# Kernel tuning notes

Measured on AMD Instinct MI355X. Metric: run time of the kernel, lower is better.

Reference implementation:

```python
import jax, jax.numpy as jnp
import numpy as np

N = 50000      # nodes
E = 800000     # edges (before self-loops)
D_IN = 256     # input feature dim
H = 4          # attention heads
C = 32         # per-head channels
HID = H * C    # 128, concat output dim
BN_EPS = 1e-5


def setup_inputs() -> dict:
    key = jax.random.key(0)
    ks = jax.random.split(key, 24)
    inp = {}
    inp["x"] = jax.random.normal(ks[0], (N, D_IN), jnp.float32)
    inp["edge_index"] = jax.random.randint(ks[1], (2, E), 0, N, jnp.int32)
    # layer 1 GATConv params
    inp["W1"] = jax.random.normal(ks[2], (D_IN, HID), jnp.float32) * (2.0 / (D_IN + HID)) ** 0.5
    inp["att_src1"] = jax.random.normal(ks[3], (H, C), jnp.float32) * 0.1
    inp["att_dst1"] = jax.random.normal(ks[4], (H, C), jnp.float32) * 0.1
    inp["bias1"] = jnp.zeros((HID,), jnp.float32)
    # layer 1 BatchNorm (eval mode)
    inp["gamma1"] = 1.0 + 0.1 * jax.random.normal(ks[5], (HID,), jnp.float32)
    inp["beta1"] = 0.1 * jax.random.normal(ks[6], (HID,), jnp.float32)
    inp["mean1"] = 0.1 * jax.random.normal(ks[7], (HID,), jnp.float32)
    inp["var1"] = 0.5 + jax.random.uniform(ks[8], (HID,), jnp.float32)
    # layer 2 GATConv params
    inp["W2"] = jax.random.normal(ks[9], (HID, HID), jnp.float32) * (2.0 / (HID + HID)) ** 0.5
    inp["att_src2"] = jax.random.normal(ks[10], (H, C), jnp.float32) * 0.1
    inp["att_dst2"] = jax.random.normal(ks[11], (H, C), jnp.float32) * 0.1
    inp["bias2"] = jnp.zeros((HID,), jnp.float32)
    # layer 2 BatchNorm (eval mode)
    inp["gamma2"] = 1.0 + 0.1 * jax.random.normal(ks[12], (HID,), jnp.float32)
    inp["beta2"] = 0.1 * jax.random.normal(ks[13], (HID,), jnp.float32)
    inp["mean2"] = 0.1 * jax.random.normal(ks[14], (HID,), jnp.float32)
    inp["var2"] = 0.5 + jax.random.uniform(ks[15], (HID,), jnp.float32)
    return inp


def _gat_layer(x, src, dst, W, att_src, att_dst, bias):
    # x: [N, D]; src/dst: [Etot] with self-loops already appended
    h = (x @ W).reshape(N, H, C)                       # [N, H, C]
    a_s = jnp.einsum("nhc,hc->nh", h, att_src)         # [N, H]
    a_d = jnp.einsum("nhc,hc->nh", h, att_dst)         # [N, H]
    e = jax.nn.leaky_relu(a_s[src] + a_d[dst], 0.2)    # [Etot, H]
    # edge softmax over incoming edges of each destination node
    m = jax.ops.segment_max(e, dst, num_segments=N)    # [N, H]
    ex = jnp.exp(e - m[dst])                           # [Etot, H]
    den = jax.ops.segment_sum(ex, dst, num_segments=N) # [N, H]
    alpha = ex / (den[dst] + 1e-16)                    # [Etot, H]
    out = jax.ops.segment_sum(h[src] * alpha[:, :, None], dst, num_segments=N)
    return out.reshape(N, HID) + bias                  # concat heads + bias


def _bn_eval(x, gamma, beta, mean, var):
    return (x - mean) * (gamma * jax.lax.rsqrt(var + BN_EPS)) + beta


def reference(x, edge_index, W1, att_src1, att_dst1, bias1, gamma1, beta1, mean1, var1,
              W2, att_src2, att_dst2, bias2, gamma2, beta2, mean2, var2):
    loop = jnp.arange(N, dtype=edge_index.dtype)
    src = jnp.concatenate([edge_index[0], loop])  # PyG GATConv adds self-loops
    dst = jnp.concatenate([edge_index[1], loop])
    h = _gat_layer(x, src, dst, W1, att_src1, att_dst1, bias1)
    h = jax.nn.relu(_bn_eval(h, gamma1, beta1, mean1, var1))  # dropout = identity (eval)
    h = _gat_layer(h, src, dst, W2, att_src2, att_dst2, bias2)
    h = jax.nn.relu(_bn_eval(h, gamma2, beta2, mean2, var2))
    return h
```

## Files before the change

### kernel.cpp

```cpp
#include <hip/hip_runtime.h>
#include <math.h>

#define N_NODES 50000
#define EDGES   800000
#define ETOT    (EDGES + N_NODES)
#define HID     128
#define NH      4

typedef __attribute__((ext_vector_type(8))) short short8;
typedef __attribute__((ext_vector_type(4))) float floatx4;

__device__ inline unsigned short f2bf(float f) {
    unsigned int u = __float_as_uint(f);
    u = u + 0x7FFFu + ((u >> 16) & 1u);
    return (unsigned short)(u >> 16);
}

#define NB 391
#define BCAP 2688
#define CHUNK 4096
#define BIN_BLOCKS ((ETOT + CHUNK - 1) / CHUNK)

__global__ __launch_bounds__(256) void init_cursor_kernel(int* __restrict__ cursor) {
    int t = blockIdx.x * 256 + threadIdx.x;
    if (t < NB) cursor[t] = t * BCAP;
}

__global__ __launch_bounds__(256) void bin_scatter_kernel(const int* __restrict__ ei,
                                                          int* __restrict__ cursor,
                                                          int* __restrict__ binned) {
    __shared__ int histL[NB];
    int t = threadIdx.x;
    for (int b = t; b < NB; b += 256) histL[b] = 0;
    __syncthreads();
    int base = blockIdx.x * CHUNK;
#pragma unroll
    for (int j = 0; j < 16; j++) {
        int e = base + j * 256 + t;
        if (e < ETOT) {
            int d = (e < EDGES) ? ei[EDGES + e] : (e - EDGES);
            atomicAdd(&histL[d >> 7], 1);
        }
    }
    __syncthreads();
    for (int b = t; b < NB; b += 256) {
        int c = histL[b];
        histL[b] = c ? atomicAdd(&cursor[b], c) : 0;
    }
    __syncthreads();
#pragma unroll
    for (int j = 0; j < 16; j++) {
        int e = base + j * 256 + t;
        if (e < ETOT) {
            int s, d;
            if (e < EDGES) { s = ei[e]; d = ei[EDGES + e]; }
            else           { s = d = e - EDGES; }
            int bb = d >> 7;
            int pos = atomicAdd(&histL[bb], 1);
            if (pos < (bb + 1) * BCAP)
                binned[pos] = (s << 7) | (d & 127);
        }
    }
}

__global__ __launch_bounds__(256) void bin_finalize_kernel(const int* __restrict__ binned,
                                                           const int* __restrict__ cursor,
                                                           int* __restrict__ starts,
                                                           int* __restrict__ degs,
                                                           int* __restrict__ csr) {
    __shared__ int histN[128];
    __shared__ int excl[128];
    int b = blockIdx.x, t = threadIdx.x;
    int n0 = b << 7;
    int S = b * BCAP;
    int cnt = cursor[b] - S;
    if (cnt > BCAP) cnt = BCAP;
    if (t < 128) histN[t] = 0;
    __syncthreads();
    for (int j = t; j < cnt; j += 256)
        atomicAdd(&histN[binned[S + j] & 127], 1);
    __syncthreads();
    int v = (t < 128) ? histN[t] : 0;
    if (t < 128) excl[t] = v;
    __syncthreads();
    for (int off = 1; off < 128; off <<= 1) {
        int x = 0, add = 0;
        if (t < 128) { x = excl[t]; if (t >= off) add = excl[t - off]; }
        __syncthreads();
        if (t < 128) excl[t] = x + add;
        __syncthreads();
    }
    if (t < 128) {
        int ex = excl[t] - v;
        int n = n0 + t;
        if (n < N_NODES) { starts[n] = S + ex; degs[n] = v; }
        histN[t] = ex;
    }
    __syncthreads();
    for (int j = t; j < cnt; j += 256) {
        int e = binned[S + j];
        int pos = atomicAdd(&histN[e & 127], 1);
        csr[S + pos] = e >> 7;
    }
}

__global__ void wtrans_coef_kernel(const float* __restrict__ W1, const float* __restrict__ W2,
                                   unsigned short* __restrict__ Wt1, unsigned short* __restrict__ Wt2,
                                   const float* __restrict__ b1, const float* __restrict__ g1,
                                   const float* __restrict__ be1, const float* __restrict__ mn1,
                                   const float* __restrict__ vr1,
                                   const float* __restrict__ b2, const float* __restrict__ g2,
                                   const float* __restrict__ be2, const float* __restrict__ mn2,
                                   const float* __restrict__ vr2, float* __restrict__ coef) {
    int i = blockIdx.x * 256 + threadIdx.x;
    if (i < 256 * 128) { int k = i >> 7, n = i & 127; Wt1[n * 256 + k] = f2bf(W1[i]); }
    if (i < 128 * 128) { int k = i >> 7, n = i & 127; Wt2[n * 128 + k] = f2bf(W2[i]); }
    if (blockIdx.x == 0) {
        int t = threadIdx.x;
        if (t < 128) {
            float sc = g1[t] * rsqrtf(vr1[t] + 1e-5f);
            coef[t]       = sc;
            coef[128 + t] = be1[t] + (b1[t] - mn1[t]) * sc;
        } else {
            int c = t - 128;
            float sc = g2[c] * rsqrtf(vr2[c] + 1e-5f);
            coef[256 + c] = sc;
            coef[384 + c] = be2[c] + (b2[c] - mn2[c]) * sc;
        }
    }
}

#define GR   64
#define KC   64
#define PADK 88
#define PADH 136

union Smem {
    struct { unsigned short Xs[GR][PADK]; unsigned short Ws[HID][PADK]; } s;
    unsigned short Hs[GR][PADH];
};

template<bool XBF16>
__global__ __launch_bounds__(256) void gemm_att_kernel(const void* __restrict__ Xv,
                                                       const unsigned short* __restrict__ Wt,
                                                       const float* __restrict__ att_src,
                                                       const float* __restrict__ att_dst,
                                                       unsigned short* __restrict__ Hout,
                                                       float* __restrict__ aS,
                                                       float* __restrict__ aD, int K) {
    __shared__ Smem sm;
    int t = threadIdx.x, lane = t & 63, w = t >> 6;
    int quad = lane >> 4, nl = lane & 15;
    int rowBase = blockIdx.x * GR;

    floatx4 acc[8];
    floatx4 zero = {0.f, 0.f, 0.f, 0.f};
#pragma unroll
    for (int b = 0; b < 8; b++) acc[b] = zero;

    const float*          Xf = (const float*)Xv;
    const unsigned short* Xb = (const unsigned short*)Xv;

    for (int k0 = 0; k0 < K; k0 += KC) {
#pragma unroll
        for (int it = 0; it < 2; it++) {
            int s5 = t + it * 256;
            int row = s5 >> 3, kg = s5 & 7;
            int gr = rowBase + row;
            unsigned short tmp[8];
            if (XBF16) {
                uint4 v = make_uint4(0, 0, 0, 0);
                if (gr < N_NODES) v = *(const uint4*)&Xb[(unsigned)(gr * K + k0 + kg * 8)];
                *(uint4*)tmp = v;
            } else {
                float4 v0 = make_float4(0, 0, 0, 0), v1 = v0;
                if (gr < N_NODES) {
                    const float* p = &Xf[(unsigned)(gr * K + k0 + kg * 8)];
                    v0 = *(const float4*)p;
                    v1 = *(const float4*)(p + 4);
                }
                tmp[0] = f2bf(v0.x); tmp[1] = f2bf(v0.y); tmp[2] = f2bf(v0.z); tmp[3] = f2bf(v0.w);
                tmp[4] = f2bf(v1.x); tmp[5] = f2bf(v1.y); tmp[6] = f2bf(v1.z); tmp[7] = f2bf(v1.w);
            }
            *(uint4*)&sm.s.Xs[row][kg * 8] = *(uint4*)tmp;
        }
#pragma unroll
        for (int it = 0; it < 4; it++) {
            int s5 = t + it * 256;
            int n = s5 >> 3, kg = s5 & 7;
            *(uint4*)&sm.s.Ws[n][kg * 8] = *(const uint4*)&Wt[(unsigned)(n * K + k0 + kg * 8)];
        }
        __syncthreads();
#pragma unroll
        for (int ks = 0; ks < 2; ks++) {
            int kb = ks * 32 + quad * 8;
            short8 a0 = *(const short8*)&sm.s.Xs[w * 16 + nl][kb];
#pragma unroll
            for (int ct = 0; ct < 8; ct++) {
                short8 b = *(const short8*)&sm.s.Ws[ct * 16 + nl][kb];
                acc[ct] = __builtin_amdgcn_mfma_f32_16x16x32_bf16(a0, b, acc[ct], 0, 0, 0);
            }
        }
        __syncthreads();
    }

#pragma unroll
    for (int ct = 0; ct < 8; ct++)
#pragma unroll
        for (int r = 0; r < 4; r++)
            sm.Hs[w * 16 + quad * 4 + r][ct * 16 + nl] = f2bf(acc[ct][r]);

    float asv[8], adv[8];
    {
        const float* ap = &att_src[nl * 8];
        const float* dp = &att_dst[nl * 8];
        *(float4*)&asv[0] = *(const float4*)ap;  *(float4*)&asv[4] = *(const float4*)(ap + 4);
        *(float4*)&adv[0] = *(const float4*)dp;  *(float4*)&adv[4] = *(const float4*)(dp + 4);
    }
    int hd = nl >> 2;
#pragma unroll
    for (int it = 0; it < 4; it++) {
        int rl = w * 16 + it * 4 + quad;
        int grow = rowBase + rl;
        uint4 v = *(const uint4*)&sm.Hs[rl][nl * 8];
        float f[8];
        f[0] = __uint_as_float(v.x << 16); f[1] = __uint_as_float(v.x & 0xffff0000u);
        f[2] = __uint_as_float(v.y << 16); f[3] = __uint_as_float(v.y & 0xffff0000u);
        f[4] = __uint_as_float(v.z << 16); f[5] = __uint_as_float(v.z & 0xffff0000u);
        f[6] = __uint_as_float(v.w << 16); f[7] = __uint_as_float(v.w & 0xffff0000u);
        float ds = 0.f, dd = 0.f;
#pragma unroll
        for (int j = 0; j < 8; j++) {
            ds = fmaf(f[j], asv[j], ds);
            dd = fmaf(f[j], adv[j], dd);
        }
        ds += __shfl_xor(ds, 1); ds += __shfl_xor(ds, 2);
        dd += __shfl_xor(dd, 1); dd += __shfl_xor(dd, 2);
        if (grow < N_NODES) {
            *(uint4*)&Hout[(unsigned)(grow * HID + nl * 8)] = v;
            if ((nl & 3) == 0) { aS[grow * 4 + hd] = ds; aD[grow * 4 + hd] = dd; }
        }
    }
}

#define ECAP 64

__device__ __forceinline__ void prefetch16(unsigned (&buf)[16], int srcreg,
                                           const char* hbase, int lane4) {
#pragma unroll
    for (int u = 0; u < 16; u++) {
        int s = __builtin_amdgcn_readlane(srcreg, u);
        buf[u] = *(const unsigned int*)(hbase + (((long)s) << 8) + lane4);
    }
}

__device__ __forceinline__ void consume16(const unsigned (&buf)[16], float xr,
                                          int abase, float& acc0, float& acc1) {
#pragma unroll
    for (int u = 0; u < 16; u++) {
        float au = __uint_as_float((unsigned)__builtin_amdgcn_ds_bpermute(
                        abase | (u << 2), (int)__float_as_uint(xr)));
        unsigned vv = buf[u];
        acc0 = fmaf(__uint_as_float(vv << 16),         au, acc0);
        acc1 = fmaf(__uint_as_float(vv & 0xffff0000u), au, acc1);
    }
}

template<bool OUTBF16>
__global__ __launch_bounds__(256) void gather_kernel(const unsigned short* __restrict__ hfeat,
                                                     const float* __restrict__ a_s,
                                                     const float* __restrict__ a_d,
                                                     const int* __restrict__ starts,
                                                     const int* __restrict__ degs,
                                                     const int* __restrict__ csr,
                                                     const float* __restrict__ coefA,
                                                     const float* __restrict__ coefB,
                                                     void* __restrict__ outv) {
    int t = threadIdx.x, lane = t & 63, ws = t >> 6;
    int h = lane >> 4, l16 = lane & 15;
    int n = blockIdx.x * 4 + ws;
    int start = starts[n];
    int deg = degs[n];
    float adh = a_d[(unsigned)(n * 4 + h)];
    int lane4 = lane << 2;
    int abase = (lane & 48) << 2;
    const char* hbase = (const char*)hfeat;

    int sreg[4];
#pragma unroll
    for (int it = 0; it < 4; it++) {
        int j = l16 + it * 16;
        sreg[it] = (j < deg) ? csr[start + j] : 0;
    }
    float e[4];
#pragma unroll
    for (int it = 0; it < 4; it++) {
        int j = l16 + it * 16;
        e[it] = -1e30f;
        if (j < deg) {
            float as = a_s[(unsigned)(sreg[it] * 4 + h)];
            float v = as + adh;
            e[it] = v > 0.f ? v : 0.2f * v;
        }
    }

    int cap = deg < ECAP ? deg : ECAP;
    unsigned vA[16], vB[16];
    prefetch16(vA, sreg[0], hbase, lane4);
    if (cap > 16) prefetch16(vB, sreg[1], hbase, lane4);

    float m = fmaxf(fmaxf(e[0], e[1]), fmaxf(e[2], e[3]));
    for (int j = ECAP + l16; j < deg; j += 16) {
        int s = csr[start + j];
        float as = a_s[(unsigned)(s * 4 + h)];
        float v = as + adh; v = v > 0.f ? v : 0.2f * v;
        m = fmaxf(m, v);
    }
#pragma unroll
    for (int off = 1; off < 16; off <<= 1) m = fmaxf(m, __shfl_xor(m, off));

    float x[4];
    float d = 0.f;
#pragma unroll
    for (int it = 0; it < 4; it++) { x[it] = __expf(e[it] - m); d += x[it]; }
    for (int j = ECAP + l16; j < deg; j += 16) {
        int s = csr[start + j];
        float as = a_s[(unsigned)(s * 4 + h)];
        float v = as + adh; v = v > 0.f ? v : 0.2f * v;
        d += __expf(v - m);
    }
#pragma unroll
    for (int off = 1; off < 16; off <<= 1) d += __shfl_xor(d, off);
    float rd = 1.0f / (d + 1e-16f);
    float xr[4];
#pragma unroll
    for (int it = 0; it < 4; it++) xr[it] = x[it] * rd;

    float acc0 = 0.f, acc1 = 0.f;
    consume16(vA, xr[0], abase, acc0, acc1);
    if (cap > 16) {
        if (cap > 32) prefetch16(vA, sreg[2], hbase, lane4);
        consume16(vB, xr[1], abase, acc0, acc1);
        if (cap > 32) {
            if (cap > 48) prefetch16(vB, sreg[3], hbase, lane4);
            consume16(vA, xr[2], abase, acc0, acc1);
            if (cap > 48) consume16(vB, xr[3], abase, acc0, acc1);
        }
    }
    for (int j = ECAP; j < deg; j++) {
        int s = csr[start + j];
        float as = a_s[(unsigned)(s * 4 + h)];
        float v2 = as + adh; v2 = v2 > 0.f ? v2 : 0.2f * v2;
        float al = __expf(v2 - m) * rd;
        unsigned int v = *(const unsigned int*)(hbase + (unsigned)((s << 8) + lane4));
        acc0 = fmaf(__uint_as_float(v << 16),         al, acc0);
        acc1 = fmaf(__uint_as_float(v & 0xffff0000u), al, acc1);
    }

    int c = lane * 2;
    float2 cA = *(const float2*)&coefA[c];
    float2 cB = *(const float2*)&coefB[c];
    float o0 = fmaxf(fmaf(acc0, cA.x, cB.x), 0.f);
    float o1 = fmaxf(fmaf(acc1, cA.y, cB.y), 0.f);
    if (OUTBF16) {
        unsigned int pk = (unsigned int)f2bf(o0) | ((unsigned int)f2bf(o1) << 16);
        ((unsigned int*)outv)[(unsigned)(n * 64 + lane)] = pk;
    } else {
        ((float2*)outv)[(unsigned)(n * 64 + lane)] = make_float2(o0, o1);
    }
}

extern "C" void kernel_launch(void* const* d_in, const int* in_sizes, int n_in,
                              void* d_out, int out_size, void* d_ws, size_t ws_size,
                              hipStream_t stream) {
    const float* x    = (const float*)d_in[0];
    const int*   ei   = (const int*)d_in[1];
    const float* W1   = (const float*)d_in[2];
    const float* as1  = (const float*)d_in[3];
    const float* ad1  = (const float*)d_in[4];
    const float* b1   = (const float*)d_in[5];
    const float* g1   = (const float*)d_in[6];
    const float* be1  = (const float*)d_in[7];
    const float* mn1  = (const float*)d_in[8];
    const float* vr1  = (const float*)d_in[9];
    const float* W2   = (const float*)d_in[10];
    const float* as2  = (const float*)d_in[11];
    const float* ad2  = (const float*)d_in[12];
    const float* b2   = (const float*)d_in[13];
    const float* g2   = (const float*)d_in[14];
    const float* be2  = (const float*)d_in[15];
    const float* mn2  = (const float*)d_in[16];
    const float* vr2  = (const float*)d_in[17];
    float* out = (float*)d_out;

    unsigned short* hb  = (unsigned short*)d_ws;
    unsigned short* x2b = hb + (size_t)N_NODES * HID;
    unsigned short* Wt1 = x2b + (size_t)N_NODES * HID;
    unsigned short* Wt2 = Wt1 + 128 * 256;
    float* aS    = (float*)(Wt2 + 128 * 128);
    float* aD    = aS + N_NODES * NH;
    float* coef  = aD + N_NODES * NH;
    int* cursor  = (int*)(coef + 512);
    int* starts  = cursor + NB;
    int* degs    = starts + N_NODES;
    int* binned  = degs + N_NODES;
    int* csr     = binned + NB * BCAP;

    init_cursor_kernel<<<2, 256, 0, stream>>>(cursor);
    bin_scatter_kernel<<<BIN_BLOCKS, 256, 0, stream>>>(ei, cursor, binned);
    bin_finalize_kernel<<<NB, 256, 0, stream>>>(binned, cursor, starts, degs, csr);
    wtrans_coef_kernel<<<128, 256, 0, stream>>>(W1, W2, Wt1, Wt2,
                                                b1, g1, be1, mn1, vr1,
                                                b2, g2, be2, mn2, vr2, coef);

    int gemmGrid = (N_NODES + GR - 1) / GR;
    int nodeGrid = N_NODES / 4;

    gemm_att_kernel<false><<<gemmGrid, 256, 0, stream>>>(x, Wt1, as1, ad1, hb, aS, aD, 256);
    gather_kernel<true><<<nodeGrid, 256, 0, stream>>>(hb, aS, aD, starts, degs, csr,
                                                      coef, coef + 128, (void*)x2b);
    gemm_att_kernel<true><<<gemmGrid, 256, 0, stream>>>(x2b, Wt2, as2, ad2, hb, aS, aD, 128);
    gather_kernel<false><<<nodeGrid, 256, 0, stream>>>(hb, aS, aD, starts, degs, csr,
                                                       coef + 256, coef + 384, (void*)out);
}
```

Baseline: 261.2 us.

## Widen gather loads to 16B, register-prefetch GEMM tiles, cache dst in binning

The gather kernel now has each lane load 16 bytes (8 bf16 channels) per source row instead of 4 bytes. Four lane-groups each handle a subset of the edges, and partial sums are combined with cross-group shuffles before the output is written. The GEMM kernel double-buffers global loads in registers so the next K-tile's loads overlap the current MFMA work. The binning kernel keeps destination indices in registers between its two passes, so they are not reloaded. These changes cut the number of memory instructions and expose latency hiding, at the cost of more registers and extra shuffle reductions.

```diff
diff --git a/kernel.cpp b/kernel.cpp
--- a/kernel.cpp
+++ b/kernel.cpp
@@ -34,13 +34,14 @@
     for (int b = t; b < NB; b += 256) histL[b] = 0;
     __syncthreads();
     int base = blockIdx.x * CHUNK;
+    int dreg[16];
 #pragma unroll
     for (int j = 0; j < 16; j++) {
         int e = base + j * 256 + t;
-        if (e < ETOT) {
-            int d = (e < EDGES) ? ei[EDGES + e] : (e - EDGES);
-            atomicAdd(&histL[d >> 7], 1);
-        }
+        int d = -1;
+        if (e < ETOT) d = (e < EDGES) ? ei[EDGES + e] : (e - EDGES);
+        dreg[j] = d;
+        if (d >= 0) atomicAdd(&histL[d >> 7], 1);
     }
     __syncthreads();
     for (int b = t; b < NB; b += 256) {
@@ -50,11 +51,10 @@
     __syncthreads();
 #pragma unroll
     for (int j = 0; j < 16; j++) {
-        int e = base + j * 256 + t;
-        if (e < ETOT) {
-            int s, d;
-            if (e < EDGES) { s = ei[e]; d = ei[EDGES + e]; }
-            else           { s = d = e - EDGES; }
+        int d = dreg[j];
+        if (d >= 0) {
+            int e = base + j * 256 + t;
+            int s = (e < EDGES) ? ei[e] : (e - EDGES);
             int bb = d >> 7;
             int pos = atomicAdd(&histL[bb], 1);
             if (pos < (bb + 1) * BCAP)
@@ -161,17 +161,20 @@
     const float*          Xf = (const float*)Xv;
     const unsigned short* Xb = (const unsigned short*)Xv;
 
-    for (int k0 = 0; k0 < K; k0 += KC) {
+    uint4  xu[2];
+    float4 xf[2][2];
+    uint4  wu[4];
+
+    auto LOADX = [&](int k0) {
 #pragma unroll
         for (int it = 0; it < 2; it++) {
             int s5 = t + it * 256;
             int row = s5 >> 3, kg = s5 & 7;
             int gr = rowBase + row;
-            unsigned short tmp[8];
             if (XBF16) {
                 uint4 v = make_uint4(0, 0, 0, 0);
                 if (gr < N_NODES) v = *(const uint4*)&Xb[(unsigned)(gr * K + k0 + kg * 8)];
-                *(uint4*)tmp = v;
+                xu[it] = v;
             } else {
                 float4 v0 = make_float4(0, 0, 0, 0), v1 = v0;
                 if (gr < N_NODES) {
@@ -179,18 +182,41 @@
                     v0 = *(const float4*)p;
                     v1 = *(const float4*)(p + 4);
                 }
+                xf[it][0] = v0; xf[it][1] = v1;
+            }
+        }
+    };
+    auto LOADW = [&](int k0) {
+#pragma unroll
+        for (int it = 0; it < 4; it++) {
+            int s5 = t + it * 256;
+            int nn = s5 >> 3, kg = s5 & 7;
+            wu[it] = *(const uint4*)&Wt[(unsigned)(nn * K + k0 + kg * 8)];
+        }
+    };
+    auto STORE = [&]() {
+#pragma unroll
+        for (int it = 0; it < 2; it++) {
+            int s5 = t + it * 256;
+            int row = s5 >> 3, kg = s5 & 7;
+            if (XBF16) {
+                *(uint4*)&sm.s.Xs[row][kg * 8] = xu[it];
+            } else {
+                unsigned short tmp[8];
+                float4 v0 = xf[it][0], v1 = xf[it][1];
                 tmp[0] = f2bf(v0.x); tmp[1] = f2bf(v0.y); tmp[2] = f2bf(v0.z); tmp[3] = f2bf(v0.w);
                 tmp[4] = f2bf(v1.x); tmp[5] = f2bf(v1.y); tmp[6] = f2bf(v1.z); tmp[7] = f2bf(v1.w);
+                *(uint4*)&sm.s.Xs[row][kg * 8] = *(uint4*)tmp;
             }
-            *(uint4*)&sm.s.Xs[row][kg * 8] = *(uint4*)tmp;
         }
 #pragma unroll
         for (int it = 0; it < 4; it++) {
             int s5 = t + it * 256;
-            int n = s5 >> 3, kg = s5 & 7;
-            *(uint4*)&sm.s.Ws[n][kg * 8] = *(const uint4*)&Wt[(unsigned)(n * K + k0 + kg * 8)];
-        }
-        __syncthreads();
+            int nn = s5 >> 3, kg = s5 & 7;
+            *(uint4*)&sm.s.Ws[nn][kg * 8] = wu[it];
+        }
+    };
+    auto MFMAC = [&]() {
 #pragma unroll
         for (int ks = 0; ks < 2; ks++) {
             int kb = ks * 32 + quad * 8;
@@ -201,8 +227,20 @@
                 acc[ct] = __builtin_amdgcn_mfma_f32_16x16x32_bf16(a0, b, acc[ct], 0, 0, 0);
             }
         }
+    };
+
+    LOADX(0); LOADW(0);
+    STORE();
+    __syncthreads();
+    for (int k0 = KC; k0 < K; k0 += KC) {
+        LOADX(k0); LOADW(k0);
+        MFMAC();
         __syncthreads();
-    }
+        STORE();
+        __syncthreads();
+    }
+    MFMAC();
+    __syncthreads();
 
 #pragma unroll
     for (int ct = 0; ct < 8; ct++)
@@ -245,24 +283,30 @@
 
 #define ECAP 64
 
-__device__ __forceinline__ void prefetch16(unsigned (&buf)[16], int srcreg,
-                                           const char* hbase, int lane4) {
-#pragma unroll
-    for (int u = 0; u < 16; u++) {
-        int s = __builtin_amdgcn_readlane(srcreg, u);
-        buf[u] = *(const unsigned int*)(hbase + (((long)s) << 8) + lane4);
-    }
-}
-
-__device__ __forceinline__ void consume16(const unsigned (&buf)[16], float xr,
-                                          int abase, float& acc0, float& acc1) {
-#pragma unroll
-    for (int u = 0; u < 16; u++) {
+__device__ __forceinline__ void prefetchR(uint4 (&buf)[4], int sregr, const char* hbase,
+                                          int sBase, int l16b) {
+#pragma unroll
+    for (int u = 0; u < 4; u++) {
+        int se = __builtin_amdgcn_ds_bpermute(sBase | (u << 2), sregr);
+        buf[u] = *(const uint4*)(hbase + (((long)se) << 8) + l16b);
+    }
+}
+
+__device__ __forceinline__ void consumeR(const uint4 (&buf)[4], float xrr, int aBase,
+                                         float (&acc)[8]) {
+#pragma unroll
+    for (int u = 0; u < 4; u++) {
         float au = __uint_as_float((unsigned)__builtin_amdgcn_ds_bpermute(
-                        abase | (u << 2), (int)__float_as_uint(xr)));
-        unsigned vv = buf[u];
-        acc0 = fmaf(__uint_as_float(vv << 16),         au, acc0);
-        acc1 = fmaf(__uint_as_float(vv & 0xffff0000u), au, acc1);
+                        aBase | (u << 2), (int)__float_as_uint(xrr)));
+        uint4 v = buf[u];
+        acc[0] = fmaf(__uint_as_float(v.x << 16),         au, acc[0]);
+        acc[1] = fmaf(__uint_as_float(v.x & 0xffff0000u), au, acc[1]);
+        acc[2] = fmaf(__uint_as_float(v.y << 16),         au, acc[2]);
+        acc[3] = fmaf(__uint_as_float(v.y & 0xffff0000u), au, acc[3]);
+        acc[4] = fmaf(__uint_as_float(v.z << 16),         au, acc[4]);
+        acc[5] = fmaf(__uint_as_float(v.z & 0xffff0000u), au, acc[5]);
+        acc[6] = fmaf(__uint_as_float(v.w << 16),         au, acc[6]);
+        acc[7] = fmaf(__uint_as_float(v.w & 0xffff0000u), au, acc[7]);
     }
 }
 
@@ -282,9 +326,10 @@
     int start = starts[n];
     int deg = degs[n];
     float adh = a_d[(unsigned)(n * 4 + h)];
-    int lane4 = lane << 2;
-    int abase = (lane & 48) << 2;
     const char* hbase = (const char*)hfeat;
+    int sBase = lane & 48;
+    int aBase = ((lane & 12) << 4) | sBase;
+    int l16b = l16 << 4;
 
     int sreg[4];
 #pragma unroll
@@ -305,9 +350,9 @@
     }
 
     int cap = deg < ECAP ? deg : ECAP;
-    unsigned vA[16], vB[16];
-    prefetch16(vA, sreg[0], hbase, lane4);
-    if (cap > 16) prefetch16(vB, sreg[1], hbase, lane4);
+    uint4 vA[4], vB[4];
+    prefetchR(vA, sreg[0], hbase, sBase, l16b);
+    if (cap > 16) prefetchR(vB, sreg[1], hbase, sBase, l16b);
 
     float m = fmaxf(fmaxf(e[0], e[1]), fmaxf(e[2], e[3]));
     for (int j = ECAP + l16; j < deg; j += 16) {
@@ -336,37 +381,64 @@
 #pragma unroll
     for (int it = 0; it < 4; it++) xr[it] = x[it] * rd;
 
-    float acc0 = 0.f, acc1 = 0.f;
-    consume16(vA, xr[0], abase, acc0, acc1);
+    float acc[8];
+#pragma unroll
+    for (int j = 0; j < 8; j++) acc[j] = 0.f;
+    consumeR(vA, xr[0], aBase, acc);
     if (cap > 16) {
-        if (cap > 32) prefetch16(vA, sreg[2], hbase, lane4);
-        consume16(vB, xr[1], abase, acc0, acc1);
+        if (cap > 32) prefetchR(vA, sreg[2], hbase, sBase, l16b);
+        consumeR(vB, xr[1], aBase, acc);
         if (cap > 32) {
-            if (cap > 48) prefetch16(vB, sreg[3], hbase, lane4);
-            consume16(vA, xr[2], abase, acc0, acc1);
-            if (cap > 48) consume16(vB, xr[3], abase, acc0, acc1);
-        }
-    }
-    for (int j = ECAP; j < deg; j++) {
-        int s = csr[start + j];
-        float as = a_s[(unsigned)(s * 4 + h)];
-        float v2 = as + adh; v2 = v2 > 0.f ? v2 : 0.2f * v2;
-        float al = __expf(v2 - m) * rd;
-        unsigned int v = *(const unsigned int*)(hbase + (unsigned)((s << 8) + lane4));
-        acc0 = fmaf(__uint_as_float(v << 16),         al, acc0);
-        acc1 = fmaf(__uint_as_float(v & 0xffff0000u), al, acc1);
-    }
-
-    int c = lane * 2;
+            if (cap > 48) prefetchR(vB, sreg[3], hbase, sBase, l16b);
+            consumeR(vA, xr[2], aBase, acc);
+            if (cap > 48) consumeR(vB, xr[3], aBase, acc);
+        }
+    }
+    if (deg > ECAP) {
+        int hh = l16 >> 2;
+        int gB = (lane & 12) << 4;
+        float mB  = __uint_as_float((unsigned)__builtin_amdgcn_ds_bpermute(gB, (int)__float_as_uint(m)));
+        float rdB = __uint_as_float((unsigned)__builtin_amdgcn_ds_bpermute(gB, (int)__float_as_uint(rd)));
+        float adhB = a_d[(unsigned)(n * 4 + hh)];
+        for (int j = ECAP; j < deg; j++) {
+            int s = csr[start + j];
+            float asv = a_s[(unsigned)(s * 4 + hh)];
+            float v2 = asv + adhB; v2 = v2 > 0.f ? v2 : 0.2f * v2;
+            float al = __expf(v2 - mB) * rdB;
+            uint4 v = *(const uint4*)(hbase + (((long)s) << 8) + l16b);
+            acc[0] = fmaf(__uint_as_float(v.x << 16),         al, acc[0]);
+            acc[1] = fmaf(__uint_as_float(v.x & 0xffff0000u), al, acc[1]);
+            acc[2] = fmaf(__uint_as_float(v.y << 16),         al, acc[2]);
+            acc[3] = fmaf(__uint_as_float(v.y & 0xffff0000u), al, acc[3]);
+            acc[4] = fmaf(__uint_as_float(v.z << 16),         al, acc[4]);
+            acc[5] = fmaf(__uint_as_float(v.z & 0xffff0000u), al, acc[5]);
+            acc[6] = fmaf(__uint_as_float(v.w << 16),         al, acc[6]);
+            acc[7] = fmaf(__uint_as_float(v.w & 0xffff0000u), al, acc[7]);
+        }
+    }
+
+#pragma unroll
+    for (int j = 0; j < 8; j++) {
+        acc[j] += __shfl_xor(acc[j], 16);
+        acc[j] += __shfl_xor(acc[j], 32);
+    }
+
+    int g = lane >> 4;
+    float o0 = acc[0], o1 = acc[1];
+    if (g == 1) { o0 = acc[2]; o1 = acc[3]; }
+    if (g == 2) { o0 = acc[4]; o1 = acc[5]; }
+    if (g == 3) { o0 = acc[6]; o1 = acc[7]; }
+    int c = (l16 << 3) + (g << 1);
     float2 cA = *(const float2*)&coefA[c];
     float2 cB = *(const float2*)&coefB[c];
-    float o0 = fmaxf(fmaf(acc0, cA.x, cB.x), 0.f);
-    float o1 = fmaxf(fmaf(acc1, cA.y, cB.y), 0.f);
+    float r0 = fmaxf(fmaf(o0, cA.x, cB.x), 0.f);
+    float r1 = fmaxf(fmaf(o1, cA.y, cB.y), 0.f);
+    unsigned oidx = (unsigned)(n * 64 + (l16 << 2) + g);
     if (OUTBF16) {
-        unsigned int pk = (unsigned int)f2bf(o0) | ((unsigned int)f2bf(o1) << 16);
-        ((unsigned int*)outv)[(unsigned)(n * 64 + lane)] = pk;
+        unsigned int pk = (unsigned int)f2bf(r0) | ((unsigned int)f2bf(r1) << 16);
+        ((unsigned int*)outv)[oidx] = pk;
     } else {
-        ((float2*)outv)[(unsigned)(n * 64 + lane)] = make_float2(o0, o1);
+        ((float2*)outv)[oidx] = make_float2(r0, r1);
     }
 }
 
```

Result: slower. 275.5 us (+5.5%).
